# Kernel tuning notes

Hardware: AMD Instinct MI355X
Metric: run time of the kernel (lower is better)

## Reference

```python
import jax, jax.numpy as jnp
import numpy as np

SEQ_LEN, BATCH, T = 128, 32, 32
START, END = 30, 31  # start_tag / end_tag from init_kwargs


def setup_inputs() -> dict:
    key = jax.random.key(0)
    k1, k2 = jax.random.split(key)
    scores = jax.random.normal(k1, (SEQ_LEN, BATCH, T, T, T), dtype=jnp.float32)
    target = jax.random.randint(k2, (SEQ_LEN, BATCH, 1), 0, T ** 3, dtype=jnp.int64)
    mask = jnp.ones((SEQ_LEN, BATCH), dtype=bool)
    return {"scores": scores, "target": target, "mask": mask}


def reference(scores, target, mask):
    seq_len, bat = scores.shape[0], scores.shape[1]

    # gold-path energy: gather flattened tag-triple score at each step, masked sum
    flat = scores.reshape(seq_len, bat, -1)                  # (S, B, T^3)
    tg = jnp.take_along_axis(flat, target, axis=2)[..., 0]   # (S, B)
    tg_energy = jnp.sum(jnp.where(mask, tg, jnp.zeros((), tg.dtype)))

    # init partition over (prev_prev=START fixed out) -> (B, T, T) over (prev, cur)
    p1 = scores[0, :, START, START, :]                       # (B, T)
    partition = p1[:, :, None] + scores[1, :, START, :, :]   # (B, T, T)

    # forward-algorithm recurrence: logsumexp out oldest tag each step
    def step(part, inp):
        s_t, m_t = inp                                       # (B,T,T,T), (B,)
        cur = s_t + part[:, :, :, None]                      # broadcast over new tag
        cp = jax.nn.logsumexp(cur, axis=1)                   # (B, T, T)
        part = jnp.where(m_t[:, None, None], cp, part)
        return part, None

    partition, _ = jax.lax.scan(step, partition, (scores[2:], mask[2:]))

    z = partition[:, END, END].sum()
    return (z - tg_energy) / bat  # average_batch=True
```

## Files before the change

kernel.cpp:

```cpp
#include <hip/hip_runtime.h>
#include <hip/hip_bf16.h>
#include <math.h>

#define SEQ_LEN 128
#define BATCH   32
#define T       32
#define TT      (T*T)
#define TTT     (T*T*T)
#define START   30
#define END     31

#define LOG2E   1.44269504088896f
#define OFF4    5.77078016355587f

typedef unsigned long long u64;

__device__ __forceinline__ u64 pt_pack(int tag, float v) {
    union { float f; unsigned int u; } c; c.f = v;
    return ((u64)(unsigned int)tag << 32) | (u64)c.u;
}
__device__ __forceinline__ float pt_val(u64 w) {
    union { unsigned int u; float f; } c; c.u = (unsigned int)w; return c.f;
}
__device__ __forceinline__ int pt_tag(u64 w) { return (int)(w >> 32); }

__device__ __forceinline__ u64 ald64(const u64* p) {
    return __hip_atomic_load(p, __ATOMIC_RELAXED, __HIP_MEMORY_SCOPE_AGENT);
}
__device__ __forceinline__ void ast64(u64* p, u64 v) {
    __hip_atomic_store(p, v, __ATOMIC_RELAXED, __HIP_MEMORY_SCOPE_AGENT);
}

#define BLOCK_SYNC() do {                                   \
    asm volatile("s_waitcnt lgkmcnt(0)" ::: "memory");      \
    __builtin_amdgcn_sched_barrier(0);                      \
    __builtin_amdgcn_s_barrier();                           \
    __builtin_amdgcn_sched_barrier(0);                      \
} while (0)

__global__ __launch_bounds__(256) void tg_kernel(const float* __restrict__ scores,
                                                 const int*   __restrict__ target,
                                                 const int*   __restrict__ mask,
                                                 float*       __restrict__ ws) {
    int idx = blockIdx.x * 256 + threadIdx.x;
    float v = 0.0f;
    if (mask[idx] != 0) v = scores[(size_t)idx * TTT + target[idx]];
    #pragma unroll
    for (int off = 32; off > 0; off >>= 1) v += __shfl_down(v, off, 64);
    __shared__ float partial[4];
    int wave = threadIdx.x >> 6, lane = threadIdx.x & 63;
    if (lane == 0) partial[wave] = v;
    __syncthreads();
    if (threadIdx.x == 0)
        ws[blockIdx.x] = partial[0] + partial[1] + partial[2] + partial[3];
}

__global__ __launch_bounds__(256) void init_dfb(const float* __restrict__ scores,
                                                u64* __restrict__ ptF,
                                                u64* __restrict__ ptB) {
    const int blk = blockIdx.x, tid = threadIdx.x;
    if (blk < BATCH) {
        const int b = blk;
        u64* pt = ptF + (size_t)b * 2048;
        #pragma unroll
        for (int q = 0; q < 4; ++q) {
            int e = q * 256 + tid;
            int i = e & 31, j = e >> 5;
            float p1 = scores[(size_t)(0*BATCH + b)*TTT + START*TT + START*T + i];
            float s1 = scores[(size_t)(1*BATCH + b)*TTT + START*TT + i*T + j];
            pt[1024 + e] = pt_pack(1, __expf(p1 + s1));
            pt[e]        = 0ULL;
        }
    } else {
        const int b = blk - BATCH;
        u64* pt = ptB + (size_t)b * 2048;
        #pragma unroll
        for (int q = 0; q < 4; ++q) {
            int e = q * 256 + tid;
            float v = (e == END*T + END) ? 1.0f : 0.0f;
            pt[e]        = pt_pack(128, v);
            pt[1024 + e] = 0ULL;
        }
    }
}

__global__ __launch_bounds__(512, 4) void scan_rd(const float* __restrict__ scores,
                                                  const int*   __restrict__ maskI,
                                                  u64*         __restrict__ ptF,
                                                  u64*         __restrict__ ptB) {
    const int bid   = blockIdx.x;
    const int g     = bid & 7;
    const int chain = bid >> 3;
    const int b     = chain & 31;
    const bool dirB = (chain >> 5) != 0;
    const int tid   = threadIdx.x;
    const int lane  = tid & 63;

    const u64 mlo = __ballot(maskI[lane * BATCH + b] != 0);
    const u64 mhi = __ballot(maskI[(64 + lane) * BATCH + b] != 0);
    auto act_of = [&](int t) {
        return (((t < 64) ? (mlo >> t) : (mhi >> (t - 64))) & 1ULL) != 0ULL;
    };

    u64* const pt = (dirB ? ptB : ptF) + (size_t)b * 2048;
    const int i0 = tid >> 5;
    const int f  = tid & 31;
    const size_t offA = (size_t)i0 * TT + g * 128 + f * 4;
    auto sb = [&](int t) { return scores + ((size_t)t * BATCH + b) * TTT; };

    if (!dirB) {
        __shared__ __align__(16) float sm[4][128 * 33];
        __shared__ __align__(16) float pld[2][128];
        const int oF = tid >> 2, s4 = tid & 3;
        const int jj = oF >> 5, k = oF & 31;
        const int jcol = 4 * g + jj;
        const int ownW = k * 32 + jcol;
        float lastval = pt_val(pt[1024 + ownW]);

        float4 X0, X1;
        auto issue = [&](int t) {
            const float* p = sb(t) + offA;
            X0 = *(const float4*)p; X1 = *(const float4*)(p + 16 * TT);
        };
        auto scat = [&](int bf) {
            #pragma unroll
            for (int q = 0; q < 4; ++q) {
                sm[bf][(f*4 + q)*33 + i0]      = (&X0.x)[q];
                sm[bf][(f*4 + q)*33 + i0 + 16] = (&X1.x)[q];
            }
        };

        issue(2); scat(2);
        issue(3); scat(3);
        issue(4);
        __syncthreads();

        for (int t = 2; t <= 64; ++t) {
            const bool act  = act_of(t);
            const int  pbuf = t & 1;
            if (t + 2 <= 64) scat((t + 2) & 3);
            if (t + 3 <= 64) issue(t + 3);
            if (tid < 64) {
                const int tagw = t - 1;
                const u64* src = pt + (size_t)((t - 1) & 1) * 1024 + 128 * g;
                u64 w0, w1; bool d0 = false, d1 = false;
                for (;;) {
                    if (!d0) { w0 = ald64(src + lane);      d0 = pt_tag(w0) == tagw; }
                    if (!d1) { w1 = ald64(src + 64 + lane); d1 = pt_tag(w1) == tagw; }
                    if (__all(d0 && d1)) break;
                }
                pld[pbuf][lane]      = pt_val(w0);
                pld[pbuf][lane + 64] = pt_val(w1);
            }
            BLOCK_SYNC();
            u64* dst = pt + (size_t)(t & 1) * 1024;
            if (act) {
                const float* row = &sm[t & 3][oF * 33 + 8 * s4];
                const float* pp  = &pld[pbuf][jj * 32 + 8 * s4];
                float acc = 0.f;
                #pragma unroll
                for (int m = 0; m < 8; ++m)
                    acc = fmaf(exp2f(fmaf(row[m], LOG2E, -OFF4)), pp[m], acc);
                acc += __shfl_xor(acc, 1, 64);
                acc += __shfl_xor(acc, 2, 64);
                if (s4 == 0) { lastval = acc; ast64(dst + ownW, pt_pack(t, acc)); }
            } else {
                if (s4 == 0) ast64(dst + ownW, pt_pack(t, lastval));
            }
        }
    } else {
        __shared__ __align__(16) float pld[2][128];
        const int jj = f >> 3, k4 = f & 7;
        const int jb = 4 * g + jj;
        const int ownW0 = i0 * 32 + jb, ownW1 = (i0 + 16) * 32 + jb;
        float last0 = pt_val(pt[ownW0]);
        float last1 = pt_val(pt[ownW1]);

        float4 A0, A1, B0, B1;
        auto issueR = [&](float4& Y0, float4& Y1, int t) {
            const float* p = sb(t) + offA;
            Y0 = *(const float4*)p; Y1 = *(const float4*)(p + 16 * TT);
        };

        auto stepB = [&](int t, const float4& X0, const float4& X1) {
            const bool act  = act_of(t);
            const int  pbuf = t & 1;
            if (tid < 64) {
                const int tagw = t + 1;
                const u64* src = pt + (size_t)((t + 1) & 1) * 1024 + 128 * g;
                u64 w0, w1; bool d0 = false, d1 = false;
                for (;;) {
                    if (!d0) { w0 = ald64(src + lane);      d0 = pt_tag(w0) == tagw; }
                    if (!d1) { w1 = ald64(src + 64 + lane); d1 = pt_tag(w1) == tagw; }
                    if (__all(d0 && d1)) break;
                }
                pld[pbuf][lane]      = pt_val(w0);
                pld[pbuf][lane + 64] = pt_val(w1);
            }
            BLOCK_SYNC();
            u64* dst = pt + (size_t)(t & 1) * 1024;
            if (act) {
                const float4 Rv = *(const float4*)&pld[pbuf][jj * 32 + 4 * k4];
                float a0, a1;
                a0 = exp2f(fmaf(X0.x, LOG2E, -OFF4)) * Rv.x;
                a0 = fmaf(exp2f(fmaf(X0.y, LOG2E, -OFF4)), Rv.y, a0);
                a0 = fmaf(exp2f(fmaf(X0.z, LOG2E, -OFF4)), Rv.z, a0);
                a0 = fmaf(exp2f(fmaf(X0.w, LOG2E, -OFF4)), Rv.w, a0);
                a1 = exp2f(fmaf(X1.x, LOG2E, -OFF4)) * Rv.x;
                a1 = fmaf(exp2f(fmaf(X1.y, LOG2E, -OFF4)), Rv.y, a1);
                a1 = fmaf(exp2f(fmaf(X1.z, LOG2E, -OFF4)), Rv.z, a1);
                a1 = fmaf(exp2f(fmaf(X1.w, LOG2E, -OFF4)), Rv.w, a1);
                a0 += __shfl_xor(a0, 1, 64); a0 += __shfl_xor(a0, 2, 64); a0 += __shfl_xor(a0, 4, 64);
                a1 += __shfl_xor(a1, 1, 64); a1 += __shfl_xor(a1, 2, 64); a1 += __shfl_xor(a1, 4, 64);
                if (k4 == 0) {
                    last0 = a0; last1 = a1;
                    ast64(dst + ownW0, pt_pack(t, a0));
                    ast64(dst + ownW1, pt_pack(t, a1));
                }
            } else {
                if (k4 == 0) {
                    ast64(dst + ownW0, pt_pack(t, last0));
                    ast64(dst + ownW1, pt_pack(t, last1));
                }
            }
        };

        issueR(A0, A1, 127);
        for (int t = 127; t >= 65; t -= 2) {
            if (t - 1 >= 65) issueR(B0, B1, t - 1);
            stepB(t, A0, A1);
            if (t - 2 >= 65) issueR(A0, A1, t - 2);
            if (t - 1 >= 65) stepB(t - 1, B0, B1);
        }
    }
}

__global__ __launch_bounds__(1024) void finalize_dfb(const float* __restrict__ ws,
                                                     const u64*  __restrict__ ptF,
                                                     const u64*  __restrict__ ptB,
                                                     const int*  __restrict__ mask,
                                                     float*      __restrict__ out) {
    __shared__ float zs[32];
    const int w = threadIdx.x >> 6, lane = threadIdx.x & 63;
    for (int rep = 0; rep < 2; ++rep) {
        const int b = w + rep * 16;
        const u64* qf = ptF + (size_t)b * 2048;
        const u64* rb = ptB + (size_t)b * 2048 + 1024;
        float dot = 0.f;
        #pragma unroll
        for (int e = 0; e < 16; ++e) {
            const int x = lane + 64 * e;
            dot += pt_val(qf[x]) * pt_val(rb[(x & 31) * 32 + (x >> 5)]);
        }
        float cnt = 0.f;
        {
            int t = 2 + lane;
            if (t < SEQ_LEN) cnt += (mask[t*BATCH + b] != 0) ? 1.f : 0.f;
            t += 64;
            if (t < SEQ_LEN) cnt += (mask[t*BATCH + b] != 0) ? 1.f : 0.f;
        }
        #pragma unroll
        for (int off = 32; off > 0; off >>= 1) {
            dot += __shfl_xor(dot, off, 64);
            cnt += __shfl_xor(cnt, off, 64);
        }
        if (lane == 0) zs[b] = 4.0f * cnt + logf(dot);
    }
    __syncthreads();
    if (threadIdx.x == 0) {
        float tg = 0.f, z = 0.f;
        #pragma unroll
        for (int i = 0; i < 16; ++i) tg += ws[i];
        #pragma unroll
        for (int i = 0; i < 32; ++i) z += zs[i];
        out[0] = (z - tg) / (float)BATCH;
    }
}

__global__ __launch_bounds__(1024) void scan_fast(const float* __restrict__ scores,
                                                  const int*   __restrict__ maskI,
                                                  float*       __restrict__ ws) {
    const int b    = blockIdx.x;
    const int tid  = threadIdx.x;
    const int w    = tid >> 6;
    const int lane = tid & 63;
    const int h    = lane >> 4;
    const int jp   = (lane >> 3) & 1;
    const int k4   = lane & 7;
    const int j    = w * 2 + jp;

    __shared__ float Q[2][TT];
    __shared__ int   lmask[SEQ_LEN];
    if (tid < SEQ_LEN) lmask[tid] = maskI[tid * BATCH + b];
    {
        int x = tid >> 5, y = tid & 31;
        float p1 = scores[(size_t)(0*BATCH + b)*TTT + START*TT + START*T + x];
        float s1 = scores[(size_t)(1*BATCH + b)*TTT + START*TT + x*T + y];
        Q[1][x*T + y] = __expf(p1 + s1);
    }
    __syncthreads();
    const int loff = h*8*TT + j*T + k4*4;
    float4 SA[8], SB[8];
    auto issue = [&](float4 (&S)[8], int t) {
        const float* p = scores + ((size_t)t*BATCH + b)*TTT + loff;
        #pragma unroll
        for (int m = 0; m < 8; ++m) S[m] = *(const float4*)(p + m*TT);
    };
    auto process = [&](float4 (&S)[8], int t) {
        const float* qc = Q[(t-1) & 1];
        float*       qn = Q[t & 1];
        #pragma unroll
        for (int m = 0; m < 8; ++m) {
            S[m].x = exp2f(fmaf(S[m].x, LOG2E, -OFF4));
            S[m].y = exp2f(fmaf(S[m].y, LOG2E, -OFF4));
            S[m].z = exp2f(fmaf(S[m].z, LOG2E, -OFF4));
            S[m].w = exp2f(fmaf(S[m].w, LOG2E, -OFF4));
        }
        float4 acc = make_float4(0.f, 0.f, 0.f, 0.f);
        #pragma unroll
        for (int m = 0; m < 8; ++m) {
            float q = qc[(h*8 + m)*T + j];
            acc.x = fmaf(S[m].x, q, acc.x);
            acc.y = fmaf(S[m].y, q, acc.y);
            acc.z = fmaf(S[m].z, q, acc.z);
            acc.w = fmaf(S[m].w, q, acc.w);
        }
        acc.x += __shfl_xor(acc.x, 16, 64); acc.y += __shfl_xor(acc.y, 16, 64);
        acc.z += __shfl_xor(acc.z, 16, 64); acc.w += __shfl_xor(acc.w, 16, 64);
        acc.x += __shfl_xor(acc.x, 32, 64); acc.y += __shfl_xor(acc.y, 32, 64);
        acc.z += __shfl_xor(acc.z, 32, 64); acc.w += __shfl_xor(acc.w, 32, 64);
        if (lane < 16) {
            if (lmask[t] != 0) *(float4*)&qn[j*T + k4*4] = acc;
            else               *(float4*)&qn[j*T + k4*4] = *(const float4*)&qc[j*T + k4*4];
        }
        asm volatile("s_waitcnt lgkmcnt(0)" ::: "memory");
        __builtin_amdgcn_s_barrier();
    };
    issue(SA, 2);
    for (int t = 2; t < SEQ_LEN; t += 2) {
        issue(SB, t + 1);
        process(SA, t);
        if (t + 2 < SEQ_LEN) issue(SA, t + 2);
        process(SB, t + 1);
    }
    if (tid == 0) {
        int cnt = 0;
        for (int t = 2; t < SEQ_LEN; ++t) cnt += (lmask[t] != 0);
        ws[16 + b] = 4.0f * (float)cnt + logf(Q[1][END*T + END]);
    }
}

__global__ void finalize_simple(const float* __restrict__ ws, float* __restrict__ out) {
    if (threadIdx.x == 0) {
        float tg = 0.f, z = 0.f;
        #pragma unroll
        for (int i = 0; i < 16; ++i) tg += ws[i];
        #pragma unroll
        for (int i = 0; i < 32; ++i) z += ws[16 + i];
        out[0] = (z - tg) / (float)BATCH;
    }
}

extern "C" void kernel_launch(void* const* d_in, const int* in_sizes, int n_in,
                              void* d_out, int out_size, void* d_ws, size_t ws_size,
                              hipStream_t stream) {
    const float* scores = (const float*)d_in[0];
    const int*   target = (const int*)d_in[1];
    const int*   mask   = (const int*)d_in[2];
    float* out = (float*)d_out;
    float* ws  = (float*)d_ws;
    u64*   ptF = (u64*)((char*)d_ws + 1024);
    u64*   ptB = ptF + (size_t)BATCH * 2048;
    const size_t need = 1024 + (size_t)2 * BATCH * 2048 * sizeof(u64);

    tg_kernel<<<16, 256, 0, stream>>>(scores, target, mask, ws);
    if (ws_size >= need) {
        init_dfb<<<2*BATCH, 256, 0, stream>>>(scores, ptF, ptB);
        scan_rd<<<512, 512, 0, stream>>>(scores, mask, ptF, ptB);
        finalize_dfb<<<1, 1024, 0, stream>>>(ws, ptF, ptB, mask, out);
    } else {
        scan_fast<<<BATCH, 1024, 0, stream>>>(scores, mask, ws);
        finalize_simple<<<1, 64, 0, stream>>>(ws, out);
    }
}
```

Measured before the change: 185.6 us.

## Fuse init and gold-score gather into scan with dedicated poller wave

Replaces the init, tg and scan kernels with one scan kernel. Each block gets a separate 64-thread polling wave plus 256 compute threads. The gold-path gather is folded into that poller wave, and the initial partition state is computed in-kernel instead of by a separate init launch. The backward direction now prefetches per-output score rows into registers with a two-step double buffer. The change cuts kernel launches and overlaps flag polling with score prefetching and scattering. In exchange it adds a memset launch and gives each block fewer compute threads with more work per thread.

```diff
diff --git a/kernel.cpp b/kernel.cpp
--- a/kernel.cpp
+++ b/kernel.cpp
@@ -37,6 +37,247 @@
     __builtin_amdgcn_s_barrier();                           \
     __builtin_amdgcn_sched_barrier(0);                      \
 } while (0)
+
+__global__ __launch_bounds__(320, 3) void scan_pi(const float* __restrict__ scores,
+                                                  const int*   __restrict__ target,
+                                                  const int*   __restrict__ maskI,
+                                                  u64*         __restrict__ ptF,
+                                                  u64*         __restrict__ ptB,
+                                                  float*       __restrict__ wsg) {
+    const int bid   = blockIdx.x;
+    const int g     = bid & 7;
+    const int chain = bid >> 3;
+    const int b     = chain & 31;
+    const bool dirB = (chain >> 5) != 0;
+    const int tid   = threadIdx.x;
+    const int lane  = tid & 63;
+
+    __shared__ __align__(16) float sm[4][128 * 33];
+    __shared__ float pld[2][128];
+
+    const u64 mlo = __ballot(maskI[lane * BATCH + b] != 0);
+    const u64 mhi = __ballot(maskI[(64 + lane) * BATCH + b] != 0);
+    auto act_of = [&](int t) {
+        return (((t < 64) ? (mlo >> t) : (mhi >> (t - 64))) & 1ULL) != 0ULL;
+    };
+
+    u64* const pt = (dirB ? ptB : ptF) + (size_t)b * 2048;
+    auto sb = [&](int t) { return scores + ((size_t)t * BATCH + b) * TTT; };
+
+    if (tid < 64) {
+        const int idx = bid * 8 + lane;
+        float tv = 0.f;
+        if (lane < 8 && maskI[idx] != 0)
+            tv = scores[(size_t)idx * TTT + target[idx]];
+        #pragma unroll
+        for (int off = 32; off > 0; off >>= 1) tv += __shfl_xor(tv, off, 64);
+        if (lane == 0) wsg[bid] = tv;
+    }
+
+    const int ct  = tid - 64;
+    const int out = ct >> 1;
+    const int h   = ct & 1;
+
+    if (!dirB) {
+        const int jj   = out >> 5, k = out & 31;
+        const int jcol = 4 * g + jj;
+        const int ownW = k * 32 + jcol;
+
+        float lastval = 0.f;
+        float4 fv[4];
+
+        auto issueT = [&](int t) {
+            const float* base = sb(t) + g * 128;
+            #pragma unroll
+            for (int n = 0; n < 4; ++n) {
+                const int p = ct + 256 * n;
+                fv[n] = *(const float4*)(base + (size_t)(p >> 5) * TT + (p & 31) * 4);
+            }
+        };
+        auto scatT = [&](int buf) {
+            #pragma unroll
+            for (int n = 0; n < 4; ++n) {
+                const int p = ct + 256 * n;
+                const int i = p >> 5, r0 = (p & 31) * 4;
+                sm[buf][(r0 + 0) * 33 + i] = fv[n].x;
+                sm[buf][(r0 + 1) * 33 + i] = fv[n].y;
+                sm[buf][(r0 + 2) * 33 + i] = fv[n].z;
+                sm[buf][(r0 + 3) * 33 + i] = fv[n].w;
+            }
+        };
+
+        if (tid >= 64) {
+            if (h == 0) {
+                float p1v = scores[(size_t)(0*BATCH + b)*TTT + START*TT + START*T + jcol];
+                float s1v = scores[(size_t)(1*BATCH + b)*TTT + START*TT + jcol*T + k];
+                lastval = __expf(p1v + s1v);
+            }
+            issueT(2); scatT(2);
+            issueT(3); scatT(3);
+            issueT(4);
+        } else {
+            const float* s0b = scores + (size_t)(0*BATCH + b)*TTT + START*TT + START*T;
+            const float* s1b = scores + (size_t)(1*BATCH + b)*TTT + START*TT;
+            const int x0 = lane, x1 = lane + 64;
+            pld[0][x0] = __expf(s0b[x0 & 31] + s1b[(x0 & 31)*T + 4*g + (x0 >> 5)]);
+            pld[0][x1] = __expf(s0b[x1 & 31] + s1b[(x1 & 31)*T + 4*g + (x1 >> 5)]);
+        }
+        __syncthreads();
+
+        for (int t = 2; t <= 64; ++t) {
+            const bool act  = act_of(t);
+            const int  pbuf = t & 1;
+            if (tid >= 64) {
+                if (t + 2 <= 64) scatT((t + 2) & 3);
+                if (t + 3 <= 64) issueT(t + 3);
+            } else if (t > 2) {
+                const int tagw = t - 1;
+                const u64* src = pt + (size_t)((t - 1) & 1) * 1024 + 128 * g;
+                u64 a0, a1; bool d0 = false, d1 = false;
+                for (;;) {
+                    if (!d0) { a0 = ald64(src + lane);      d0 = pt_tag(a0) == tagw; }
+                    if (!d1) { a1 = ald64(src + 64 + lane); d1 = pt_tag(a1) == tagw; }
+                    if (__all(d0 && d1)) break;
+                }
+                pld[pbuf][lane]      = pt_val(a0);
+                pld[pbuf][lane + 64] = pt_val(a1);
+            }
+            BLOCK_SYNC();
+            if (tid >= 64) {
+                u64* dst = pt + (size_t)(t & 1) * 1024;
+                if (act) {
+                    const float* row = &sm[t & 3][out * 33 + 16 * h];
+                    const float* pp  = &pld[pbuf][jj * 32 + 16 * h];
+                    float acc = 0.f;
+                    #pragma unroll
+                    for (int m = 0; m < 16; ++m)
+                        acc = fmaf(exp2f(fmaf(row[m], LOG2E, -OFF4)), pp[m], acc);
+                    acc += __shfl_xor(acc, 1, 64);
+                    if (h == 0) { lastval = acc; ast64(dst + ownW, pt_pack(t, acc)); }
+                } else {
+                    if (h == 0) ast64(dst + ownW, pt_pack(t, lastval));
+                }
+            }
+        }
+    } else {
+        const int i   = out >> 2, jjB = out & 3;
+        const int jb  = 4 * g + jjB;
+        const int ownW = i * 32 + jb;
+        float lastval = (i == END && jb == END) ? 1.0f : 0.0f;
+
+        float4 EA[4], EB[4];
+        auto issueE = [&](float4* E, int t) {
+            const float* p = sb(t) + (size_t)i * TT + jb * 32 + 16 * h;
+            E[0] = *(const float4*)(p + 0);
+            E[1] = *(const float4*)(p + 4);
+            E[2] = *(const float4*)(p + 8);
+            E[3] = *(const float4*)(p + 12);
+        };
+        auto pollB = [&](int t) {
+            const int tagw = t + 1;
+            const u64* src = pt + (size_t)((t + 1) & 1) * 1024 + 128 * g;
+            u64 a0, a1; bool d0 = false, d1 = false;
+            for (;;) {
+                if (!d0) { a0 = ald64(src + lane);      d0 = pt_tag(a0) == tagw; }
+                if (!d1) { a1 = ald64(src + 64 + lane); d1 = pt_tag(a1) == tagw; }
+                if (__all(d0 && d1)) break;
+            }
+            pld[t & 1][lane]      = pt_val(a0);
+            pld[t & 1][lane + 64] = pt_val(a1);
+        };
+        auto computeB = [&](int t, const float4* E) {
+            const bool act  = act_of(t);
+            const int  pbuf = t & 1;
+            u64* dst = pt + (size_t)(t & 1) * 1024;
+            if (act) {
+                const float* pp = &pld[pbuf][jjB * 32 + 16 * h];
+                float acc = 0.f;
+                #pragma unroll
+                for (int n = 0; n < 4; ++n) {
+                    acc = fmaf(exp2f(fmaf(E[n].x, LOG2E, -OFF4)), pp[n*4 + 0], acc);
+                    acc = fmaf(exp2f(fmaf(E[n].y, LOG2E, -OFF4)), pp[n*4 + 1], acc);
+                    acc = fmaf(exp2f(fmaf(E[n].z, LOG2E, -OFF4)), pp[n*4 + 2], acc);
+                    acc = fmaf(exp2f(fmaf(E[n].w, LOG2E, -OFF4)), pp[n*4 + 3], acc);
+                }
+                acc += __shfl_xor(acc, 1, 64);
+                if (h == 0) { lastval = acc; ast64(dst + ownW, pt_pack(t, acc)); }
+            } else {
+                if (h == 0) ast64(dst + ownW, pt_pack(t, lastval));
+            }
+        };
+
+        if (tid >= 64) issueE(EA, 127);
+        else {
+            const int x0 = lane, x1 = lane + 64;
+            pld[1][x0] = (4*g + (x0 >> 5) == END && (x0 & 31) == END) ? 1.f : 0.f;
+            pld[1][x1] = (4*g + (x1 >> 5) == END && (x1 & 31) == END) ? 1.f : 0.f;
+        }
+        __syncthreads();
+
+        for (int t = 127; t >= 65; t -= 2) {
+            if (tid >= 64 && t - 1 >= 65) issueE(EB, t - 1);
+            if (tid < 64 && t < 127) pollB(t);
+            BLOCK_SYNC();
+            if (tid >= 64) computeB(t, EA);
+            if (t - 1 < 65) break;
+            if (tid >= 64 && t - 2 >= 65) issueE(EA, t - 2);
+            if (tid < 64) pollB(t - 1);
+            BLOCK_SYNC();
+            if (tid >= 64) computeB(t - 1, EB);
+        }
+    }
+}
+
+__global__ __launch_bounds__(1024) void finalize_pi(const float* __restrict__ wsg,
+                                                    const u64*  __restrict__ ptF,
+                                                    const u64*  __restrict__ ptB,
+                                                    const int*  __restrict__ mask,
+                                                    float*      __restrict__ out) {
+    __shared__ float zs[32];
+    __shared__ float tgp[8];
+    const int w = threadIdx.x >> 6, lane = threadIdx.x & 63;
+
+    {
+        float tv = (threadIdx.x < 512) ? wsg[threadIdx.x] : 0.f;
+        #pragma unroll
+        for (int off = 32; off > 0; off >>= 1) tv += __shfl_xor(tv, off, 64);
+        if (lane == 0 && w < 8) tgp[w] = tv;
+    }
+
+    for (int rep = 0; rep < 2; ++rep) {
+        const int b = w + rep * 16;
+        const u64* qf = ptF + (size_t)b * 2048;
+        const u64* rb = ptB + (size_t)b * 2048 + 1024;
+        float dot = 0.f;
+        #pragma unroll
+        for (int e = 0; e < 16; ++e) {
+            const int x = lane + 64 * e;
+            dot += pt_val(qf[x]) * pt_val(rb[(x & 31) * 32 + (x >> 5)]);
+        }
+        float cnt = 0.f;
+        {
+            int t = 2 + lane;
+            if (t < SEQ_LEN) cnt += (mask[t*BATCH + b] != 0) ? 1.f : 0.f;
+            t += 64;
+            if (t < SEQ_LEN) cnt += (mask[t*BATCH + b] != 0) ? 1.f : 0.f;
+        }
+        #pragma unroll
+        for (int off = 32; off > 0; off >>= 1) {
+            dot += __shfl_xor(dot, off, 64);
+            cnt += __shfl_xor(cnt, off, 64);
+        }
+        if (lane == 0) zs[b] = 4.0f * cnt + logf(dot);
+    }
+    __syncthreads();
+    if (threadIdx.x == 0) {
+        float tg = 0.f, z = 0.f;
+        #pragma unroll
+        for (int i = 0; i < 8; ++i) tg += tgp[i];
+        #pragma unroll
+        for (int i = 0; i < 32; ++i) z += zs[i];
+        out[0] = (z - tg) / (float)BATCH;
+    }
+}
 
 __global__ __launch_bounds__(256) void tg_kernel(const float* __restrict__ scores,
                                                  const int*   __restrict__ target,
@@ -55,228 +296,6 @@
         ws[blockIdx.x] = partial[0] + partial[1] + partial[2] + partial[3];
 }
 
-__global__ __launch_bounds__(256) void init_dfb(const float* __restrict__ scores,
-                                                u64* __restrict__ ptF,
-                                                u64* __restrict__ ptB) {
-    const int blk = blockIdx.x, tid = threadIdx.x;
-    if (blk < BATCH) {
-        const int b = blk;
-        u64* pt = ptF + (size_t)b * 2048;
-        #pragma unroll
-        for (int q = 0; q < 4; ++q) {
-            int e = q * 256 + tid;
-            int i = e & 31, j = e >> 5;
-            float p1 = scores[(size_t)(0*BATCH + b)*TTT + START*TT + START*T + i];
-            float s1 = scores[(size_t)(1*BATCH + b)*TTT + START*TT + i*T + j];
-            pt[1024 + e] = pt_pack(1, __expf(p1 + s1));
-            pt[e]        = 0ULL;
-        }
-    } else {
-        const int b = blk - BATCH;
-        u64* pt = ptB + (size_t)b * 2048;
-        #pragma unroll
-        for (int q = 0; q < 4; ++q) {
-            int e = q * 256 + tid;
-            float v = (e == END*T + END) ? 1.0f : 0.0f;
-            pt[e]        = pt_pack(128, v);
-            pt[1024 + e] = 0ULL;
-        }
-    }
-}
-
-__global__ __launch_bounds__(512, 4) void scan_rd(const float* __restrict__ scores,
-                                                  const int*   __restrict__ maskI,
-                                                  u64*         __restrict__ ptF,
-                                                  u64*         __restrict__ ptB) {
-    const int bid   = blockIdx.x;
-    const int g     = bid & 7;
-    const int chain = bid >> 3;
-    const int b     = chain & 31;
-    const bool dirB = (chain >> 5) != 0;
-    const int tid   = threadIdx.x;
-    const int lane  = tid & 63;
-
-    const u64 mlo = __ballot(maskI[lane * BATCH + b] != 0);
-    const u64 mhi = __ballot(maskI[(64 + lane) * BATCH + b] != 0);
-    auto act_of = [&](int t) {
-        return (((t < 64) ? (mlo >> t) : (mhi >> (t - 64))) & 1ULL) != 0ULL;
-    };
-
-    u64* const pt = (dirB ? ptB : ptF) + (size_t)b * 2048;
-    const int i0 = tid >> 5;
-    const int f  = tid & 31;
-    const size_t offA = (size_t)i0 * TT + g * 128 + f * 4;
-    auto sb = [&](int t) { return scores + ((size_t)t * BATCH + b) * TTT; };
-
-    if (!dirB) {
-        __shared__ __align__(16) float sm[4][128 * 33];
-        __shared__ __align__(16) float pld[2][128];
-        const int oF = tid >> 2, s4 = tid & 3;
-        const int jj = oF >> 5, k = oF & 31;
-        const int jcol = 4 * g + jj;
-        const int ownW = k * 32 + jcol;
-        float lastval = pt_val(pt[1024 + ownW]);
-
-        float4 X0, X1;
-        auto issue = [&](int t) {
-            const float* p = sb(t) + offA;
-            X0 = *(const float4*)p; X1 = *(const float4*)(p + 16 * TT);
-        };
-        auto scat = [&](int bf) {
-            #pragma unroll
-            for (int q = 0; q < 4; ++q) {
-                sm[bf][(f*4 + q)*33 + i0]      = (&X0.x)[q];
-                sm[bf][(f*4 + q)*33 + i0 + 16] = (&X1.x)[q];
-            }
-        };
-
-        issue(2); scat(2);
-        issue(3); scat(3);
-        issue(4);
-        __syncthreads();
-
-        for (int t = 2; t <= 64; ++t) {
-            const bool act  = act_of(t);
-            const int  pbuf = t & 1;
-            if (t + 2 <= 64) scat((t + 2) & 3);
-            if (t + 3 <= 64) issue(t + 3);
-            if (tid < 64) {
-                const int tagw = t - 1;
-                const u64* src = pt + (size_t)((t - 1) & 1) * 1024 + 128 * g;
-                u64 w0, w1; bool d0 = false, d1 = false;
-                for (;;) {
-                    if (!d0) { w0 = ald64(src + lane);      d0 = pt_tag(w0) == tagw; }
-                    if (!d1) { w1 = ald64(src + 64 + lane); d1 = pt_tag(w1) == tagw; }
-                    if (__all(d0 && d1)) break;
-                }
-                pld[pbuf][lane]      = pt_val(w0);
-                pld[pbuf][lane + 64] = pt_val(w1);
-            }
-            BLOCK_SYNC();
-            u64* dst = pt + (size_t)(t & 1) * 1024;
-            if (act) {
-                const float* row = &sm[t & 3][oF * 33 + 8 * s4];
-                const float* pp  = &pld[pbuf][jj * 32 + 8 * s4];
-                float acc = 0.f;
-                #pragma unroll
-                for (int m = 0; m < 8; ++m)
-                    acc = fmaf(exp2f(fmaf(row[m], LOG2E, -OFF4)), pp[m], acc);
-                acc += __shfl_xor(acc, 1, 64);
-                acc += __shfl_xor(acc, 2, 64);
-                if (s4 == 0) { lastval = acc; ast64(dst + ownW, pt_pack(t, acc)); }
-            } else {
-                if (s4 == 0) ast64(dst + ownW, pt_pack(t, lastval));
-            }
-        }
-    } else {
-        __shared__ __align__(16) float pld[2][128];
-        const int jj = f >> 3, k4 = f & 7;
-        const int jb = 4 * g + jj;
-        const int ownW0 = i0 * 32 + jb, ownW1 = (i0 + 16) * 32 + jb;
-        float last0 = pt_val(pt[ownW0]);
-        float last1 = pt_val(pt[ownW1]);
-
-        float4 A0, A1, B0, B1;
-        auto issueR = [&](float4& Y0, float4& Y1, int t) {
-            const float* p = sb(t) + offA;
-            Y0 = *(const float4*)p; Y1 = *(const float4*)(p + 16 * TT);
-        };
-
-        auto stepB = [&](int t, const float4& X0, const float4& X1) {
-            const bool act  = act_of(t);
-            const int  pbuf = t & 1;
-            if (tid < 64) {
-                const int tagw = t + 1;
-                const u64* src = pt + (size_t)((t + 1) & 1) * 1024 + 128 * g;
-                u64 w0, w1; bool d0 = false, d1 = false;
-                for (;;) {
-                    if (!d0) { w0 = ald64(src + lane);      d0 = pt_tag(w0) == tagw; }
-                    if (!d1) { w1 = ald64(src + 64 + lane); d1 = pt_tag(w1) == tagw; }
-                    if (__all(d0 && d1)) break;
-                }
-                pld[pbuf][lane]      = pt_val(w0);
-                pld[pbuf][lane + 64] = pt_val(w1);
-            }
-            BLOCK_SYNC();
-            u64* dst = pt + (size_t)(t & 1) * 1024;
-            if (act) {
-                const float4 Rv = *(const float4*)&pld[pbuf][jj * 32 + 4 * k4];
-                float a0, a1;
-                a0 = exp2f(fmaf(X0.x, LOG2E, -OFF4)) * Rv.x;
-                a0 = fmaf(exp2f(fmaf(X0.y, LOG2E, -OFF4)), Rv.y, a0);
-                a0 = fmaf(exp2f(fmaf(X0.z, LOG2E, -OFF4)), Rv.z, a0);
-                a0 = fmaf(exp2f(fmaf(X0.w, LOG2E, -OFF4)), Rv.w, a0);
-                a1 = exp2f(fmaf(X1.x, LOG2E, -OFF4)) * Rv.x;
-                a1 = fmaf(exp2f(fmaf(X1.y, LOG2E, -OFF4)), Rv.y, a1);
-                a1 = fmaf(exp2f(fmaf(X1.z, LOG2E, -OFF4)), Rv.z, a1);
-                a1 = fmaf(exp2f(fmaf(X1.w, LOG2E, -OFF4)), Rv.w, a1);
-                a0 += __shfl_xor(a0, 1, 64); a0 += __shfl_xor(a0, 2, 64); a0 += __shfl_xor(a0, 4, 64);
-                a1 += __shfl_xor(a1, 1, 64); a1 += __shfl_xor(a1, 2, 64); a1 += __shfl_xor(a1, 4, 64);
-                if (k4 == 0) {
-                    last0 = a0; last1 = a1;
-                    ast64(dst + ownW0, pt_pack(t, a0));
-                    ast64(dst + ownW1, pt_pack(t, a1));
-                }
-            } else {
-                if (k4 == 0) {
-                    ast64(dst + ownW0, pt_pack(t, last0));
-                    ast64(dst + ownW1, pt_pack(t, last1));
-                }
-            }
-        };
-
-        issueR(A0, A1, 127);
-        for (int t = 127; t >= 65; t -= 2) {
-            if (t - 1 >= 65) issueR(B0, B1, t - 1);
-            stepB(t, A0, A1);
-            if (t - 2 >= 65) issueR(A0, A1, t - 2);
-            if (t - 1 >= 65) stepB(t - 1, B0, B1);
-        }
-    }
-}
-
-__global__ __launch_bounds__(1024) void finalize_dfb(const float* __restrict__ ws,
-                                                     const u64*  __restrict__ ptF,
-                                                     const u64*  __restrict__ ptB,
-                                                     const int*  __restrict__ mask,
-                                                     float*      __restrict__ out) {
-    __shared__ float zs[32];
-    const int w = threadIdx.x >> 6, lane = threadIdx.x & 63;
-    for (int rep = 0; rep < 2; ++rep) {
-        const int b = w + rep * 16;
-        const u64* qf = ptF + (size_t)b * 2048;
-        const u64* rb = ptB + (size_t)b * 2048 + 1024;
-        float dot = 0.f;
-        #pragma unroll
-        for (int e = 0; e < 16; ++e) {
-            const int x = lane + 64 * e;
-            dot += pt_val(qf[x]) * pt_val(rb[(x & 31) * 32 + (x >> 5)]);
-        }
-        float cnt = 0.f;
-        {
-            int t = 2 + lane;
-            if (t < SEQ_LEN) cnt += (mask[t*BATCH + b] != 0) ? 1.f : 0.f;
-            t += 64;
-            if (t < SEQ_LEN) cnt += (mask[t*BATCH + b] != 0) ? 1.f : 0.f;
-        }
-        #pragma unroll
-        for (int off = 32; off > 0; off >>= 1) {
-            dot += __shfl_xor(dot, off, 64);
-            cnt += __shfl_xor(cnt, off, 64);
-        }
-        if (lane == 0) zs[b] = 4.0f * cnt + logf(dot);
-    }
-    __syncthreads();
-    if (threadIdx.x == 0) {
-        float tg = 0.f, z = 0.f;
-        #pragma unroll
-        for (int i = 0; i < 16; ++i) tg += ws[i];
-        #pragma unroll
-        for (int i = 0; i < 32; ++i) z += zs[i];
-        out[0] = (z - tg) / (float)BATCH;
-    }
-}
-
 __global__ __launch_bounds__(1024) void scan_fast(const float* __restrict__ scores,
                                                   const int*   __restrict__ maskI,
                                                   float*       __restrict__ ws) {
@@ -369,16 +388,18 @@
     const int*   mask   = (const int*)d_in[2];
     float* out = (float*)d_out;
     float* ws  = (float*)d_ws;
-    u64*   ptF = (u64*)((char*)d_ws + 1024);
+    float* wsg = ws + 32;
+    u64*   ptF = (u64*)((char*)d_ws + 4096);
     u64*   ptB = ptF + (size_t)BATCH * 2048;
-    const size_t need = 1024 + (size_t)2 * BATCH * 2048 * sizeof(u64);
-
-    tg_kernel<<<16, 256, 0, stream>>>(scores, target, mask, ws);
+    const size_t ptBytes = (size_t)2 * BATCH * 2048 * sizeof(u64);
+    const size_t need = 4096 + ptBytes;
+
     if (ws_size >= need) {
-        init_dfb<<<2*BATCH, 256, 0, stream>>>(scores, ptF, ptB);
-        scan_rd<<<512, 512, 0, stream>>>(scores, mask, ptF, ptB);
-        finalize_dfb<<<1, 1024, 0, stream>>>(ws, ptF, ptB, mask, out);
+        hipMemsetAsync((void*)ptF, 0, ptBytes, stream);
+        scan_pi<<<512, 320, 0, stream>>>(scores, target, mask, ptF, ptB, wsg);
+        finalize_pi<<<1, 1024, 0, stream>>>(wsg, ptF, ptB, mask, out);
     } else {
+        tg_kernel<<<16, 256, 0, stream>>>(scores, target, mask, ws);
         scan_fast<<<BATCH, 1024, 0, stream>>>(scores, mask, ws);
         finalize_simple<<<1, 64, 0, stream>>>(ws, out);
     }
```

Result: slower. 281.0 us (+51.4%).
